# Performance work log

Measured on AMD Instinct MI355X. Metric: run time of the kernel, lower is better.

The kernel has to match this reference:

```python
import jax, jax.numpy as jnp
import numpy as np

DIM = 64; NH = 8; WS = 8; B = 8; H = 128; W = 128
HD = DIM // NH
SCALE = HD ** -0.5
BN_S = np.float32(1.0 / np.sqrt(1.0 + 1e-5))  # eval-mode BatchNorm with running mean=0, var=1


def conv2d(x, w, stride=1, padding=0, groups=1, bias=None):
    out = jax.lax.conv_general_dilated(
        x, w, (stride, stride), [(padding, padding), (padding, padding)],
        dimension_numbers=('NCHW', 'OIHW', 'NCHW'), feature_group_count=groups)
    if bias is not None:
        out = out + bias[None, :, None, None]
    return out


def bn(x, g, b):
    return x * (g * BN_S)[None, :, None, None] + b[None, :, None, None]


def maxpool(x, k, s):
    return jax.lax.reduce_window(x, -jnp.inf, jax.lax.max, (1, 1, k, k), (1, 1, s, s), 'VALID')


def avgpool(x, kh, kw, ph, pw):
    # torch AvgPool2d: zero padding, count_include_pad=True -> divide by full kernel size
    s = jax.lax.reduce_window(x, 0.0, jax.lax.add, (1, 1, kh, kw), (1, 1, 1, 1),
                              [(0, 0), (0, 0), (ph, ph), (pw, pw)])
    return s / (kh * kw)


def fft_h(x):
    # high-pass: zero magnitude within radius 40 of the shifted spectrum center
    h, w = x.shape[-2], x.shape[-1]
    f = jnp.fft.fftshift(jnp.fft.fft2(x), axes=(-2, -1))
    ii = jnp.arange(h)[:, None] - h // 2
    jj = jnp.arange(w)[None, :] - w // 2
    mask = (jnp.sqrt((ii * ii + jj * jj).astype(jnp.float32)) > 40.0).astype(x.dtype)
    filt = f * (jnp.abs(f) * mask)
    return jnp.abs(jnp.fft.ifft2(jnp.fft.ifftshift(filt, axes=(-2, -1))))


def gabor_branch(x, f_cos, f_sin, gb_b1, gb_b2, gb_w, w_post, g_post, b_post,
                 w_gc, b_gc, w_gc1, b_gc1, w_gc2, b_gc2):
    xs = x.shape[2]  # x_size (square input assumed, as in the torch code)
    xc = jnp.concatenate([conv2d(x, f_cos, bias=gb_b1), conv2d(x, f_sin, bias=gb_b2)], axis=1)
    wts = jax.nn.relu(gb_w)
    fw = wts / (jnp.sum(wts) + 1e-8)
    xc = fw[0] * fft_h(xc) + fw[1] * xc
    xc = jnp.clip(bn(conv2d(xc, w_post, padding=1), g_post, b_post), 0.0, 6.0)  # ReLU6
    xc = maxpool(xc, 2, 1)
    xc = jax.nn.relu(conv2d(xc, w_gc, stride=2, bias=b_gc))
    xc = maxpool(xc, 2, 2)
    xc = jax.image.resize(xc, (xc.shape[0], xc.shape[1], xs, xs), method='bilinear')
    xc = jax.nn.relu(conv2d(xc, w_gc1, padding=1, bias=b_gc1))
    xc = conv2d(xc, w_gc2, bias=b_gc2)
    return jax.nn.log_softmax(xc, axis=1)


def forward(x, w_qkv, w_l1, g_l1, b_l1, w_l2, g_l2, b_l2, f_cos, f_sin, gb_b1, gb_b2, gb_w,
            w_post, g_post, b_post, w_gc, b_gc, w_gc1, b_gc1, w_gc2, b_gc2,
            rpb_table, w_dw, g_proj, b_proj, w_pw, rel_index):
    b, c, hh, ww = x.shape
    # local branch
    local = bn(conv2d(x, w_l2), g_l2, b_l2) + bn(conv2d(x, w_l1, padding=1), g_l1, b_l1)
    local = gabor_branch(local, f_cos, f_sin, gb_b1, gb_b2, gb_w, w_post, g_post, b_post,
                         w_gc, b_gc, w_gc1, b_gc1, w_gc2, b_gc2)
    # global branch (H, W multiples of WS -> self.pad is a no-op)
    qkv = conv2d(x, w_qkv)  # [b, 3C, H, W]
    gh, gw = hh // WS, ww // WS
    t = qkv.reshape(b, 3, NH, HD, gh, WS, gw, WS)
    t = t.transpose(1, 0, 4, 6, 2, 5, 7, 3).reshape(3, b * gh * gw, NH, WS * WS, HD)
    q, k, v = t[0], t[1], t[2]
    rpb = rpb_table[rel_index.reshape(-1)].reshape(WS * WS, WS * WS, NH).transpose(2, 0, 1)
    dots = jnp.einsum('bhid,bhjd->bhij', q, k) * SCALE + rpb[None]
    attn = jax.nn.softmax(dots, axis=-1)
    o = jnp.einsum('bhij,bhjd->bhid', attn, v)
    o = o.reshape(b, gh, gw, NH, WS, WS, HD).transpose(0, 3, 6, 1, 4, 2, 5).reshape(b, c, hh, ww)
    # directional reflect-pad + avg pool (kernel (8,1)/(1,8), stride 1, pad 3)
    ox = avgpool(jnp.pad(o, ((0, 0), (0, 0), (0, 1), (0, 0)), mode='reflect'), WS, 1, WS // 2 - 1, 0)
    oy = avgpool(jnp.pad(o, ((0, 0), (0, 0), (0, 0), (0, 1)), mode='reflect'), 1, WS, 0, WS // 2 - 1)
    out = ox + oy + local
    out = jnp.pad(out, ((0, 0), (0, 0), (0, 1), (0, 1)))  # pad_out
    out = conv2d(bn(conv2d(out, w_dw, padding=(WS - 1) // 2, groups=c), g_proj, b_proj), w_pw)
    return out[:, :, :hh, :ww]


def _gabor(sig, th, lam, psi, gam, ks, use_cos):
    half = (ks - 1) // 2
    y, x = np.meshgrid(np.arange(-half, half + 1), np.arange(-half, half + 1))
    x = x.astype(np.float32); y = y.astype(np.float32)
    sx = sig[..., None, None]; sy = (sig / gam)[..., None, None]
    t = th[..., None, None]; l = lam[..., None, None]; p = psi[..., None, None]
    xt = x * np.cos(t) + y * np.sin(t)
    yt = -x * np.sin(t) + y * np.cos(t)
    env = np.exp(-0.5 * (xt ** 2 / sx ** 2 + yt ** 2 / sy ** 2))
    car = np.cos(2.0 * np.pi / l * xt + p) if use_cos else np.sin(2.0 * np.pi / l * xt + p)
    return (env * car).astype(np.float32)


def setup_inputs() -> dict:
    rng = np.random.default_rng(0)
    def rn(*s, sc=0.05):
        return jnp.asarray(rng.standard_normal(s).astype(np.float32) * sc)
    sig, th, lam, psi, gam = [rng.standard_normal((DIM // 2, DIM)).astype(np.float32) for _ in range(5)]
    f_cos = jnp.asarray(_gabor(sig, th, lam, psi, gam, 3, True))
    f_sin = jnp.asarray(_gabor(sig, th, lam, psi, gam, 3, False))
    coords = np.stack(np.meshgrid(np.arange(WS), np.arange(WS), indexing='ij')).reshape(2, -1)
    rel = (coords[:, :, None] - coords[:, None, :]).transpose(1, 2, 0)
    rel[:, :, 0] += WS - 1; rel[:, :, 1] += WS - 1; rel[:, :, 0] *= 2 * WS - 1
    rel_index = jnp.asarray(rel.sum(-1).astype(np.int32))  # [64, 64]
    return dict(
        x=rn(B, DIM, H, W, sc=1.0),
        w_qkv=rn(3 * DIM, DIM, 1, 1),
        w_l1=rn(DIM, DIM, 3, 3), g_l1=jnp.ones(DIM), b_l1=jnp.zeros(DIM),
        w_l2=rn(DIM, DIM, 1, 1), g_l2=jnp.ones(DIM), b_l2=jnp.zeros(DIM),
        f_cos=f_cos, f_sin=f_sin,
        gb_b1=rn(DIM // 2), gb_b2=rn(DIM // 2), gb_w=jnp.ones(2),
        w_post=rn(DIM, DIM, 3, 3), g_post=jnp.ones(DIM), b_post=jnp.zeros(DIM),
        w_gc=rn(64, 64, 3, 3), b_gc=rn(64),
        w_gc1=rn(64, 64, 3, 3), b_gc1=rn(64),
        w_gc2=rn(64, 64, 1, 1), b_gc2=rn(64),
        rpb_table=rn((2 * WS - 1) ** 2, NH, sc=0.02),
        w_dw=rn(DIM, 1, WS, WS), g_proj=jnp.ones(DIM), b_proj=jnp.zeros(DIM),
        w_pw=rn(DIM, DIM, 1, 1),
        rel_index=rel_index,
    )


def reference(x, w_qkv, w_l1, g_l1, b_l1, w_l2, g_l2, b_l2, f_cos, f_sin, gb_b1, gb_b2, gb_w,
              w_post, g_post, b_post, w_gc, b_gc, w_gc1, b_gc1, w_gc2, b_gc2,
              rpb_table, w_dw, g_proj, b_proj, w_pw, rel_index):
    return forward(x, w_qkv, w_l1, g_l1, b_l1, w_l2, g_l2, b_l2, f_cos, f_sin, gb_b1, gb_b2, gb_w,
                   w_post, g_post, b_post, w_gc, b_gc, w_gc1, b_gc1, w_gc2, b_gc2,
                   rpb_table, w_dw, g_proj, b_proj, w_pw, rel_index)
```

## Files before the change

### kernel.cpp

```cpp
#include <hip/hip_runtime.h>
#include <math.h>

#define BN_SC 0.9999950000375f
#define P2N   (6.283185307179586f / 126.f)
#define ATT_SCALE 0.35355339059327373f

typedef float v4f __attribute__((ext_vector_type(4)));
typedef short bf16x8 __attribute__((ext_vector_type(8)));
typedef float f32x4 __attribute__((ext_vector_type(4)));
typedef unsigned short u16;

enum { M_LOCAL = 0, M_GABOR = 1, M_BNRELU6 = 2, M_BIASRELU = 3 };

__device__ __forceinline__ u16 f2bf(float f) {
  unsigned u = __float_as_uint(f);
  return (u16)((u + 0x7FFFu + ((u >> 16) & 1u)) >> 16);
}
__device__ __forceinline__ float bf2f(u16 h) {
  return __uint_as_float(((unsigned)h) << 16);
}

__global__ __launch_bounds__(256) void rpbprep_k(
    const float* __restrict__ rpb, const int* __restrict__ relidx, float* __restrict__ rpbt)
{
// ... 263 lines not shown
  const int wco = wv & 1, wpx = wv >> 1;
  const int b = blockIdx.y;
  const int oy0 = (blockIdx.x >> 3) * 8, ox0 = (blockIdx.x & 7) * 8;
  const int l15 = lane & 15, l4 = lane >> 4;
  const int pr_ = l15 >> 3, pc_ = l15 & 7;
  const int aoff = l15 * 576 + l4 * 8;
  const u16* wh0 = wh + wco * 32 * 576 + aoff;
  const u16* wl0 = wl + wco * 32 * 576 + aoff;

  f32x4 acc[2][2];
#pragma unroll
  for (int f = 0; f < 2; ++f)
#pragma unroll
    for (int g = 0; g < 2; ++g) { f32x4 z = {0.f, 0.f, 0.f, 0.f}; acc[f][g] = z; }

  const int PHA[9] = {0, 0, 0, 0, 1, 1, 2, 2, 3};
  const int OYO[9] = {0, 0, 1, 1, 0, 1, 0, 0, 0};
  const int OXO[9] = {0, 1, 0, 1, 0, 0, 0, 1, 0};

#pragma unroll 1
  for (int cc = 0; cc < 64; cc += 32) {
#pragma unroll
    for (int pos = 0; pos < 9; ++pos) {
      const int ph = PHA[pos];
      if (pos == 0 || pos == 4 || pos == 6 || pos == 8) {
        __syncthreads();
        for (int e = tid; e < 648; e += 256) {
          int pix = e >> 3, part = e & 7;
          int pu = pix / 9, pv = pix - pu * 9;
          int u = oy0 + pu, v = ox0 + pv;
          uint4 val = make_uint4(0u, 0u, 0u, 0u);
          if (u < 63 && v < 63) {
            const u16* s = ((part < 4) ? ph_h : ph_l)
                + (((size_t)(b * 4 + ph) * 63 + u) * 63 + v) * 64 + cc + (part & 3) * 8;
            val = *(const uint4*)s;
          }
          *(uint4*)(lds + pix * 144 + part * 16) = val;
        }
        __syncthreads();
      }
      bf16x8 ah0 = *(const bf16x8*)(wh0 + pos * 64 + cc);
      bf16x8 al0 = *(const bf16x8*)(wl0 + pos * 64 + cc);
      bf16x8 ah1 = *(const bf16x8*)(wh0 + 16 * 576 + pos * 64 + cc);
      bf16x8 al1 = *(const bf16x8*)(wl0 + 16 * 576 + pos * 64 + cc);
#pragma unroll
      for (int g = 0; g < 2; ++g) {
        const int lrow = wpx * 4 + g * 2 + pr_ + OYO[pos];
        const int lcol = pc_ + OXO[pos];
        const char* pb = lds + (lrow * 9 + lcol) * 144 + l4 * 16;
        bf16x8 bh = *(const bf16x8*)pb;
        bf16x8 bl = *(const bf16x8*)(pb + 64);
        acc[0][g] = __builtin_amdgcn_mfma_f32_16x16x32_bf16(ah0, bh, acc[0][g], 0, 0, 0);
        acc[1][g] = __builtin_amdgcn_mfma_f32_16x16x32_bf16(ah1, bh, acc[1][g], 0, 0, 0);
        acc[0][g] = __builtin_amdgcn_mfma_f32_16x16x32_bf16(ah0, bl, acc[0][g], 0, 0, 0);
        acc[0][g] = __builtin_amdgcn_mfma_f32_16x16x32_bf16(al0, bh, acc[0][g], 0, 0, 0);
        acc[1][g] = __builtin_amdgcn_mfma_f32_16x16x32_bf16(ah1, bl, acc[1][g], 0, 0, 0);
        acc[1][g] = __builtin_amdgcn_mfma_f32_16x16x32_bf16(al1, bh, acc[1][g], 0, 0, 0);
      }
    }
  }

  const int ox = ox0 + pc_;
#pragma unroll
  for (int f = 0; f < 2; ++f) {
    const int cb = wco * 32 + f * 16 + l4 * 4;
#pragma unroll
    for (int g = 0; g < 2; ++g) {
      int oy = oy0 + wpx * 4 + g * 2 + pr_;
      if (oy >= 62 || ox >= 62) continue;
#pragma unroll
      for (int j = 0; j < 4; ++j) {
        float v = acc[f][g][j] + bias[cb + j];
        out[(((size_t)(b * 64) + cb + j) * 62 + oy) * 62 + ox] = fmaxf(v, 0.f);
      }
    }
  }
}


__global__ __launch_bounds__(256)
void dft_rows_fwd_mf(const float* __restrict__ in, float* __restrict__ outC,
                     const u16* __restrict__ th, const u16* __restrict__ tl, int planeBase)
{
  __shared__ char lds[64 * 528];
  const int tid = threadIdx.x;
  const int lane = tid & 63;
  const int wv = __builtin_amdgcn_readfirstlane(tid >> 6);
  const int l15 = lane & 15, l4 = lane >> 4;
  const int lp = blockIdx.x >> 1, rb = (blockIdx.x & 1) * 64;
  const float* src = in + (size_t)(planeBase + lp) * 15876;

  for (int e = tid; e < 8192; e += 256) {
    int row = e >> 7, k = e & 127;
    int gr = rb + row;
    float v = (gr < 126 && k < 126) ? src[(size_t)gr * 126 + k] : 0.f;
    u16 h = f2bf(v);
    char* p = lds + row * 528 + k * 2;
    *(u16*)p = h;
    *(u16*)(p + 256) = f2bf(v - bf2f(h));
  }
  __syncthreads();

  f32x4 acc[8];
#pragma unroll
  for (int nf = 0; nf < 8; ++nf) { f32x4 z = {0.f, 0.f, 0.f, 0.f}; acc[nf] = z; }
#pragma unroll
  for (int cc = 0; cc < 128; cc += 32) {
    const char* pb = lds + (wv * 16 + l15) * 528 + cc * 2 + l4 * 16;
    bf16x8 bh = *(const bf16x8*)pb;
    bf16x8 bl = *(const bf16x8*)(pb + 256);
#pragma unroll
    for (int nf = 0; nf < 8; ++nf) {
      const int ao = (nf * 16 + l15) * 128 + cc + l4 * 8;
      bf16x8 ah = *(const bf16x8*)(th + ao);
      bf16x8 al = *(const bf16x8*)(tl + ao);
      acc[nf] = __builtin_amdgcn_mfma_f32_16x16x32_bf16(ah, bh, acc[nf], 0, 0, 0);
      acc[nf] = __builtin_amdgcn_mfma_f32_16x16x32_bf16(ah, bl, acc[nf], 0, 0, 0);
      acc[nf] = __builtin_amdgcn_mfma_f32_16x16x32_bf16(al, bh, acc[nf], 0, 0, 0);
    }
  }
  const int row = rb + wv * 16 + l15;
  if (row < 126) {
    float* o = outC + (size_t)lp * 16128 + (size_t)row * 128;
#pragma unroll
    for (int nf = 0; nf < 8; ++nf)
      *(f32x4*)(o + nf * 16 + l4 * 4) = acc[nf];
  }
}

template<bool FWD>
__global__ __launch_bounds__(256)
void dft_cols_mf(const float* __restrict__ inC, float* __restrict__ outC,
                 const u16* __restrict__ tch, const u16* __restrict__ tcl,
                 const u16* __restrict__ tsh, const u16* __restrict__ tsl)
{
  __shared__ char lds[33792];
  const int tid = threadIdx.x;
  const int lane = tid & 63;
  const int wv = __builtin_amdgcn_readfirstlane(tid >> 6);
  const int l15 = lane & 15, l4 = lane >> 4;
  const int lp = blockIdx.x >> 1, gbase = (blockIdx.x & 1) * 32;
  const float2* src = (const float2*)(inC + (size_t)lp * 16128);

  for (int e = tid; e < 4096; e += 256) {
    int col = e >> 7, k = e & 127;
    float2 v = make_float2(0.f, 0.f);
    if (k < 126) v = src[k * 64 + gbase + col];
    u16 hr = f2bf(v.x);
    u16 hi2 = f2bf(v.y);
    char* pr = lds + col * 528 + k * 2;
    char* pi = lds + 16896 + col * 528 + k * 2;
    *(u16*)pr = hr;        *(u16*)(pr + 256) = f2bf(v.x - bf2f(hr));
    *(u16*)pi = hi2;       *(u16*)(pi + 256) = f2bf(v.y - bf2f(hi2));
  }
  __syncthreads();

  f32x4 aRc[2][2], aRs[2][2], aIc[2][2], aIs[2][2];
#pragma unroll
  for (int a = 0; a < 2; ++a)
#pragma unroll
    for (int c = 0; c < 2; ++c) {
      f32x4 z = {0.f, 0.f, 0.f, 0.f};
      aRc[a][c] = z; aRs[a][c] = z; aIc[a][c] = z; aIs[a][c] = z;
    }

#pragma unroll
  for (int cc = 0; cc < 128; cc += 32) {
    bf16x8 brh[2], brl[2], bih[2], bil[2];
#pragma unroll
    for (int cf = 0; cf < 2; ++cf) {
      const char* pr = lds + (cf * 16 + l15) * 528 + cc * 2 + l4 * 16;
      brh[cf] = *(const bf16x8*)pr;
      brl[cf] = *(const bf16x8*)(pr + 256);
      const char* pi = lds + 16896 + (cf * 16 + l15) * 528 + cc * 2 + l4 * 16;
      bih[cf] = *(const bf16x8*)pi;
      bil[cf] = *(const bf16x8*)(pi + 256);
    }
#pragma unroll
    for (int chf = 0; chf < 2; ++chf) {
      const int ao = (wv * 32 + chf * 16 + l15) * 128 + cc + l4 * 8;
      bf16x8 ach = *(const bf16x8*)(tch + ao);
      bf16x8 acl = *(const bf16x8*)(tcl + ao);
      bf16x8 ash = *(const bf16x8*)(tsh + ao);
      bf16x8 asl = *(const bf16x8*)(tsl + ao);
#pragma unroll
      for (int cf = 0; cf < 2; ++cf) {
        aRc[chf][cf] = __builtin_amdgcn_mfma_f32_16x16x32_bf16(ach, brh[cf], aRc[chf][cf], 0, 0, 0);
        aRc[chf][cf] = __builtin_amdgcn_mfma_f32_16x16x32_bf16(ach, brl[cf], aRc[chf][cf], 0, 0, 0);
        aRc[chf][cf] = __builtin_amdgcn_mfma_f32_16x16x32_bf16(acl, brh[cf], aRc[chf][cf], 0, 0, 0);
        aRs[chf][cf] = __builtin_amdgcn_mfma_f32_16x16x32_bf16(ash, bih[cf], aRs[chf][cf], 0, 0, 0);
        aRs[chf][cf] = __builtin_amdgcn_mfma_f32_16x16x32_bf16(ash, bil[cf], aRs[chf][cf], 0, 0, 0);
        aRs[chf][cf] = __builtin_amdgcn_mfma_f32_16x16x32_bf16(asl, bih[cf], aRs[chf][cf], 0, 0, 0);
        aIc[chf][cf] = __builtin_amdgcn_mfma_f32_16x16x32_bf16(ach, bih[cf], aIc[chf][cf], 0, 0, 0);
        aIc[chf][cf] = __builtin_amdgcn_mfma_f32_16x16x32_bf16(ach, bil[cf], aIc[chf][cf], 0, 0, 0);
        aIc[chf][cf] = __builtin_amdgcn_mfma_f32_16x16x32_bf16(acl, bih[cf], aIc[chf][cf], 0, 0, 0);
        aIs[chf][cf] = __builtin_amdgcn_mfma_f32_16x16x32_bf16(ash, brh[cf], aIs[chf][cf], 0, 0, 0);
        aIs[chf][cf] = __builtin_amdgcn_mfma_f32_16x16x32_bf16(ash, brl[cf], aIs[chf][cf], 0, 0, 0);
        aIs[chf][cf] = __builtin_amdgcn_mfma_f32_16x16x32_bf16(asl, brh[cf], aIs[chf][cf], 0, 0, 0);
      }
    }
  }

  float2* dst = (float2*)(outC + (size_t)lp * 16128);
#pragma unroll
  for (int chf = 0; chf < 2; ++chf)
#pragma unroll
    for (int cf = 0; cf < 2; ++cf) {
      const int col = gbase + cf * 16 + l15;
      const int chb = wv * 32 + chf * 16 + l4 * 4;
#pragma unroll
      for (int j = 0; j < 4; ++j) {
        int ch = chb + j;
        if (ch >= 126) continue;
        float Cr, Ci;
        if (FWD) { Cr = aRc[chf][cf][j] + aRs[chf][cf][j]; Ci = aIc[chf][cf][j] - aIs[chf][cf][j]; }
        else     { Cr = aRc[chf][cf][j] - aRs[chf][cf][j]; Ci = aIc[chf][cf][j] + aIs[chf][cf][j]; }
        if (FWD) {
          int f1 = (ch <= 62) ? ch : ch - 126;
          int f2 = (col <= 62) ? col : col - 126;
          float sa = (f1 * f1 + f2 * f2 > 1600)
                       ? sqrtf(Cr * Cr + Ci * Ci) * (1.f / 15876.f) : 0.f;
          Cr *= sa; Ci *= sa;
        }
        dst[(size_t)ch * 64 + col] = make_float2(Cr, Ci);
      }
    }
}

__global__ __launch_bounds__(256)
void dft_rows_inv_mix_mf(const float* __restrict__ inC, const float* __restrict__ xc0,
                         const float* __restrict__ gb_w,
                         const u16* __restrict__ th, const u16* __restrict__ tl,
                         float* __restrict__ out, int planeBase)
{
  __shared__ char lds[64 * 528];
  const int tid = threadIdx.x;
  const int lane = tid & 63;
  const int wv = __builtin_amdgcn_readfirstlane(tid >> 6);
  const int l15 = lane & 15, l4 = lane >> 4;
  const int lp = blockIdx.x >> 1, rb = (blockIdx.x & 1) * 64;
  const float* src = inC + (size_t)lp * 16128;

  for (int e = tid; e < 8192; e += 256) {
    int row = e >> 7, k = e & 127;
    int gr = rb + row;
    float v = (gr < 126) ? src[(size_t)gr * 128 + k] : 0.f;
    u16 h = f2bf(v);
    char* p = lds + row * 528 + k * 2;
    *(u16*)p = h;
    *(u16*)(p + 256) = f2bf(v - bf2f(h));
  }
  __syncthreads();

  f32x4 acc[8];
#pragma unroll
  for (int nf = 0; nf < 8; ++nf) { f32x4 z = {0.f, 0.f, 0.f, 0.f}; acc[nf] = z; }
#pragma unroll
  for (int cc = 0; cc < 128; cc += 32) {
    const char* pb = lds + (wv * 16 + l15) * 528 + cc * 2 + l4 * 16;
    bf16x8 bh = *(const bf16x8*)pb;
    bf16x8 bl = *(const bf16x8*)(pb + 256);
#pragma unroll
    for (int nf = 0; nf < 8; ++nf) {
      const int ao = (nf * 16 + l15) * 128 + cc + l4 * 8;
      bf16x8 ah = *(const bf16x8*)(th + ao);
      bf16x8 al = *(const bf16x8*)(tl + ao);
      acc[nf] = __builtin_amdgcn_mfma_f32_16x16x32_bf16(ah, bh, acc[nf], 0, 0, 0);
      acc[nf] = __builtin_amdgcn_mfma_f32_16x16x32_bf16(ah, bl, acc[nf], 0, 0, 0);
      acc[nf] = __builtin_amdgcn_mfma_f32_16x16x32_bf16(al, bh, acc[nf], 0, 0, 0);
    }
  }
  const int row = rb + wv * 16 + l15;
  if (row < 126) {
    float w0 = fmaxf(gb_w[0], 0.f), w1 = fmaxf(gb_w[1], 0.f);
    float iv = 1.f / (w0 + w1 + 1e-8f);
    const float w0i = w0 * iv, w1i = w1 * iv;
    size_t base = (size_t)(planeBase + lp) * 15876 + (size_t)row * 126;
#pragma unroll
    for (int nf = 0; nf < 8; ++nf) {
      const int n20 = nf * 16 + l4 * 4;
#pragma unroll
      for (int j = 0; j < 4; ++j) {
        int n2 = n20 + j;
        if (n2 < 126)
          out[base + n2] = w0i * fabsf(acc[nf][j]) + w1i * xc0[base + n2];
      }
    }
  }
}

__global__ __launch_bounds__(256) void mp2_k(const float* __restrict__ in, float* __restrict__ out)
{
  int idx = blockIdx.x * 256 + threadIdx.x;
  if (idx >= 512 * 31 * 31) return;
  int x = idx % 31, y = (idx / 31) % 31, p = idx / 961;
  const float* ip = in + (size_t)p * 3844 + (size_t)(2 * y) * 62 + 2 * x;
  out[idx] = fmaxf(fmaxf(ip[0], ip[1]), fmaxf(ip[62], ip[63]));
}

__global__ __launch_bounds__(256)
void resize_bf_k(const float* __restrict__ in, u16* __restrict__ xh, u16* __restrict__ xl)
{
  int idx = blockIdx.x * 256 + threadIdx.x;
  if (idx >= 2097152) return;
  int cg = idx & 15, x = (idx >> 4) & 127, y = (idx >> 11) & 127, b = idx >> 18;
  float sy = (y + 0.5f) * (31.f / 128.f) - 0.5f; sy = fminf(fmaxf(sy, 0.f), 30.f);
  float sx = (x + 0.5f) * (31.f / 128.f) - 0.5f; sx = fminf(fmaxf(sx, 0.f), 30.f);
  int y0 = (int)sy; float fy = sy - (float)y0; int y1 = min(y0 + 1, 30);
  int x0 = (int)sx; float fx = sx - (float)x0; int x1 = min(x0 + 1, 30);
  const float* base = in + (size_t)(b * 64 + cg * 4) * 961;
  ushort4 hv, lv;
#pragma unroll
  for (int k = 0; k < 4; ++k) {
    const float* ip = base + k * 961;
    float v = (1.f - fy) * ((1.f - fx) * ip[y0 * 31 + x0] + fx * ip[y0 * 31 + x1])
            + fy         * ((1.f - fx) * ip[y1 * 31 + x0] + fx * ip[y1 * 31 + x1]);
    u16 h = f2bf(v);
    ((u16*)&hv)[k] = h;
    ((u16*)&lv)[k] = f2bf(v - bf2f(h));
  }
  size_t o = (((size_t)b * 128 + y) * 128 + x) * 64 + cg * 4;
  *(ushort4*)(xh + o) = hv;
  *(ushort4*)(xl + o) = lv;
}

__global__ __launch_bounds__(256)
void pwlsm_mf(const u16* __restrict__ xh, const u16* __restrict__ xl,
              const u16* __restrict__ wh, const u16* __restrict__ wl,
              const float* __restrict__ bias, float* __restrict__ out)
{
  __shared__ char lds[17664];
  const int tid = threadIdx.x;
  const int lane = tid & 63;
  const int wv = __builtin_amdgcn_readfirstlane(tid >> 6);
  const int l15 = lane & 15, l4 = lane >> 4;
  const size_t px0 = (size_t)blockIdx.x * 64;

  for (int e = tid; e < 1024; e += 256) {
    int pix = e >> 4, part = e & 15;
    const u16* s = ((part < 8) ? xh : xl) + (px0 + pix) * 64 + (part & 7) * 8;
    char* d = lds + pix * 272 + ((part < 8) ? part * 16 : 128 + (part - 8) * 16);
    *(uint4*)d = *(const uint4*)s;
  }
  __syncthreads();

  f32x4 acc[4];
#pragma unroll
  for (int p = 0; p < 4; ++p) { f32x4 z = {0.f, 0.f, 0.f, 0.f}; acc[p] = z; }
  const int co16 = wv * 16;
  const u16* wa = wh + (size_t)(co16 + l15) * 64 + l4 * 8;
  const u16* wb = wl + (size_t)(co16 + l15) * 64 + l4 * 8;
#pragma unroll
  for (int cc = 0; cc < 64; cc += 32) {
    bf16x8 ah = *(const bf16x8*)(wa + cc);
    bf16x8 al = *(const bf16x8*)(wb + cc);
#pragma unroll
    for (int p = 0; p < 4; ++p) {
      const char* pb = lds + (16 * p + l15) * 272 + cc * 2 + l4 * 16;
      bf16x8 bh = *(const bf16x8*)pb;
      bf16x8 bl = *(const bf16x8*)(pb + 128);
      acc[p] = __builtin_amdgcn_mfma_f32_16x16x32_bf16(ah, bh, acc[p], 0, 0, 0);
      acc[p] = __builtin_amdgcn_mfma_f32_16x16x32_bf16(ah, bl, acc[p], 0, 0, 0);
      acc[p] = __builtin_amdgcn_mfma_f32_16x16x32_bf16(al, bh, acc[p], 0, 0, 0);
    }
  }
  float4 bv = *(const float4*)&bias[co16 + l4 * 4];
  __syncthreads();
  float* zs = (float*)lds;
// ... 77 lines not shown
void attn_mf_k(const float* __restrict__ x, const u16* __restrict__ wqh,
               const u16* __restrict__ wql, const float* __restrict__ rpbt,
               float* __restrict__ o_out)
{
  __shared__ uint4 lds4[3200];
  char* lds = (char*)lds4;
  const int tid = threadIdx.x;
  const int lane = tid & 63;
  const int wv = __builtin_amdgcn_readfirstlane(tid >> 6);
  const int b = blockIdx.x >> 8, gy = (blockIdx.x >> 4) & 15, gx = blockIdx.x & 15;
  const int y0 = gy * 8, x0 = gx * 8;
  const int l15 = lane & 15, l4 = lane >> 4;

  for (int e = tid; e < 4096; e += 256) {
    int cin = e >> 6, pix = e & 63;
    float v = x[((size_t)(b * 64 + cin) * 128 + (y0 + (pix >> 3))) * 128 + x0 + (pix & 7)];
    u16 h = f2bf(v);
    *(u16*)(lds + pix * 272 + cin * 2)       = h;
    *(u16*)(lds + pix * 272 + 128 + cin * 2) = f2bf(v - bf2f(h));
  }
  __syncthreads();

  f32x4 acc[3][4];
#pragma unroll
  for (int r = 0; r < 3; ++r)
#pragma unroll
    for (int p = 0; p < 4; ++p) { f32x4 z = {0.f, 0.f, 0.f, 0.f}; acc[r][p] = z; }
  const u16* wa = wqh + (size_t)(48 * wv + l15) * 64 + l4 * 8;
  const u16* wb = wql + (size_t)(48 * wv + l15) * 64 + l4 * 8;
#pragma unroll
  for (int cc = 0; cc < 64; cc += 32) {
    bf16x8 bh[4], bl[4];
#pragma unroll
    for (int p = 0; p < 4; ++p) {
      const char* pb = lds + (16 * p + l15) * 272 + cc * 2 + l4 * 16;
      bh[p] = *(const bf16x8*)pb;
      bl[p] = *(const bf16x8*)(pb + 128);
    }
#pragma unroll
    for (int r = 0; r < 3; ++r) {
      bf16x8 ah = *(const bf16x8*)(wa + r * 1024 + cc);
      bf16x8 al = *(const bf16x8*)(wb + r * 1024 + cc);
#pragma unroll
      for (int p = 0; p < 4; ++p) {
        acc[r][p] = __builtin_amdgcn_mfma_f32_16x16x32_bf16(ah, bh[p], acc[r][p], 0, 0, 0);
        acc[r][p] = __builtin_amdgcn_mfma_f32_16x16x32_bf16(ah, bl[p], acc[r][p], 0, 0, 0);
        acc[r][p] = __builtin_amdgcn_mfma_f32_16x16x32_bf16(al, bh[p], acc[r][p], 0, 0, 0);
      }
    }
  }
  __syncthreads();

#pragma unroll
  for (int r = 0; r < 3; ++r) {
    const int ch0 = 48 * wv + 16 * r + l4 * 4;
#pragma unroll
    for (int p = 0; p < 4; ++p) {
      const int pix = 16 * p + l15;
      if (ch0 < 64) {
#pragma unroll
        for (int j = 0; j < 4; ++j)
          *(float*)(lds + ((ch0 + j) * 65 + pix) * 4) = acc[r][p][j];
      } else {
        const int col = (ch0 < 128) ? (ch0 - 64) : (64 + ch0 - 128);
        *(f32x4*)(lds + 17408 + pix * 528 + col * 4) = acc[r][p];
      }
    }
  }
  __syncthreads();

  const int row = y0 + (lane >> 3), col = x0 + (lane & 7);
  const int h0 = wv, h1 = wv + 4;
  float q0[8], q1[8];
#pragma unroll
  for (int d = 0; d < 8; ++d) {
    q0[d] = *(const float*)(lds + ((h0 * 8 + d) * 65 + lane) * 4);
    q1[d] = *(const float*)(lds + ((h1 * 8 + d) * 65 + lane) * 4);
  }
  const float* rb0 = rpbt + h0 * 4096;
  const float* rb1 = rpbt + h1 * 4096;
  float P0[64], P1[64];
#pragma unroll
  for (int j = 0; j < 64; ++j) { P0[j] = rb0[j * 64 + lane]; P1[j] = rb1[j * 64 + lane]; }
  float m0 = -1e30f, m1 = -1e30f;
#pragma unroll
  for (int j = 0; j < 64; ++j) {
    const char* kp = lds + 17408 + j * 528;
    float4 a0 = *(const float4*)(kp + (h0 * 8) * 4);
    float4 a1 = *(const float4*)(kp + (h0 * 8) * 4 + 16);
    float4 b0 = *(const float4*)(kp + (h1 * 8) * 4);
    float4 b1 = *(const float4*)(kp + (h1 * 8) * 4 + 16);
    float s0 = q0[0] * a0.x + q0[1] * a0.y + q0[2] * a0.z + q0[3] * a0.w
             + q0[4] * a1.x + q0[5] * a1.y + q0[6] * a1.z + q0[7] * a1.w;
    float s1 = q1[0] * b0.x + q1[1] * b0.y + q1[2] * b0.z + q1[3] * b0.w
             + q1[4] * b1.x + q1[5] * b1.y + q1[6] * b1.z + q1[7] * b1.w;
    s0 = s0 * ATT_SCALE + P0[j];
    s1 = s1 * ATT_SCALE + P1[j];
    P0[j] = s0; P1[j] = s1;
    m0 = fmaxf(m0, s0); m1 = fmaxf(m1, s1);
  }
  float sum0 = 0.f, sum1 = 0.f;
#pragma unroll
  for (int j = 0; j < 64; ++j) {
    float p0 = __expf(P0[j] - m0); P0[j] = p0; sum0 += p0;
    float p1 = __expf(P1[j] - m1); P1[j] = p1; sum1 += p1;
  }
  float inv0 = 1.f / sum0, inv1 = 1.f / sum1;

  float acc0[8], acc1[8];
#pragma unroll
  for (int d = 0; d < 8; ++d) { acc0[d] = 0.f; acc1[d] = 0.f; }
#pragma unroll
  for (int j = 0; j < 64; ++j) {
    const char* vp = lds + 17408 + j * 528 + 256;
    float p0 = P0[j], p1 = P1[j];
    float4 v00 = *(const float4*)(vp + (h0 * 8) * 4);
    float4 v01 = *(const float4*)(vp + (h0 * 8) * 4 + 16);
    float4 v10 = *(const float4*)(vp + (h1 * 8) * 4);
    float4 v11 = *(const float4*)(vp + (h1 * 8) * 4 + 16);
    acc0[0] += p0 * v00.x; acc0[1] += p0 * v00.y; acc0[2] += p0 * v00.z; acc0[3] += p0 * v00.w;
    acc0[4] += p0 * v01.x; acc0[5] += p0 * v01.y; acc0[6] += p0 * v01.z; acc0[7] += p0 * v01.w;
    acc1[0] += p1 * v10.x; acc1[1] += p1 * v10.y; acc1[2] += p1 * v10.z; acc1[3] += p1 * v10.w;
    acc1[4] += p1 * v11.x; acc1[5] += p1 * v11.y; acc1[6] += p1 * v11.z; acc1[7] += p1 * v11.w;
  }
#pragma unroll
  for (int d = 0; d < 8; ++d) {
    o_out[((size_t)(b * 64 + h0 * 8 + d) * 128 + row) * 128 + col] = acc0[d] * inv0;
    o_out[((size_t)(b * 64 + h1 * 8 + d) * 128 + row) * 128 + col] = acc1[d] * inv1;
  }
}

__global__ __launch_bounds__(256)
void avgadd_k(const float* __restrict__ o, const float* __restrict__ loc, float* __restrict__ out)
{
  __shared__ float t[24][128];
  const int tid = threadIdx.x;
  const int y0 = blockIdx.x * 16;
  const size_t p = blockIdx.y;
  const float* op = o + (p << 14);
  for (int e = tid; e < 24 * 128; e += 256) {
    int rr = e >> 7, x = e & 127;
    int r = y0 - 3 + rr;
    float v = 0.f;
    if (r >= 0 && r <= 128) { int r2 = (r == 128) ? 126 : r; v = op[r2 * 128 + x]; }
    t[rr][x] = v;
  }
  __syncthreads();
#pragma unroll
  for (int k = 0; k < 8; ++k) {
    int idx = k * 256 + tid;
    int ly = idx >> 7, x = idx & 127;
    float s1 = 0.f;
#pragma unroll
    for (int tt = 0; tt < 8; ++tt) s1 += t[ly + tt][x];
    float s2 = 0.f;
#pragma unroll
    for (int tt = 0; tt < 8; ++tt) {
      int cc = x - 3 + tt;
      if (cc >= 0 && cc <= 128) { int ss = (cc == 128) ? 126 : cc; s2 += t[ly + 3][ss]; }
    }
    size_t gi = (p << 14) + (size_t)(y0 + ly) * 128 + x;
    out[gi] = 0.125f * (s1 + s2) + loc[gi];
  }
}

__global__ __launch_bounds__(256)
void dw_k(const float* __restrict__ in, const float* __restrict__ w,
          const float* __restrict__ g, const float* __restrict__ bb, float* __restrict__ out)
{
  __shared__ float t[23 * 23];
  const int tid = threadIdx.x;
  const int tx = tid & 15, ty = tid >> 4;
  const int x0 = blockIdx.x * 16, y0 = blockIdx.y * 16;
  const int pc = blockIdx.z;
  const int c = pc & 63;
  const float* ip = in + (size_t)pc * 16384;
  for (int e = tid; e < 529; e += 256) {
    int yy = e / 23, xx = e % 23;
    int iy = y0 + yy - 3, ix = x0 + xx - 3;
    t[e] = (iy >= 0 && iy < 128 && ix >= 0 && ix < 128) ? ip[iy * 128 + ix] : 0.f;
  }
  __syncthreads();
  const float* wk = w + c * 64;
  float s = 0.f;
#pragma unroll
  for (int ky = 0; ky < 8; ++ky)
#pragma unroll
    for (int kx = 0; kx < 8; ++kx)
      s += t[(ty + ky) * 23 + tx + kx] * wk[ky * 8 + kx];
  out[(size_t)pc * 16384 + (y0 + ty) * 128 + x0 + tx] = s * (g[c] * BN_SC) + bb[c];
}

extern "C" void kernel_launch(void* const* d_in, const int* in_sizes, int n_in,
                              void* d_out, int out_size, void* d_ws, size_t ws_size,
                              hipStream_t stream)
{
  const float* x      = (const float*)d_in[0];
  const float* w_qkv  = (const float*)d_in[1];
  const float* w_l1   = (const float*)d_in[2];
  const float* g_l1   = (const float*)d_in[3];
  const float* b_l1   = (const float*)d_in[4];
  const float* w_l2   = (const float*)d_in[5];
  const float* g_l2   = (const float*)d_in[6];
  const float* b_l2   = (const float*)d_in[7];
  const float* f_cos  = (const float*)d_in[8];
  const float* f_sin  = (const float*)d_in[9];
  const float* gb_b1  = (const float*)d_in[10];
  const float* gb_b2  = (const float*)d_in[11];
  const float* gb_w   = (const float*)d_in[12];
  const float* w_post = (const float*)d_in[13];
  const float* g_post = (const float*)d_in[14];
  const float* b_post = (const float*)d_in[15];
  const float* w_gc   = (const float*)d_in[16];
  const float* b_gc   = (const float*)d_in[17];
  const float* w_gc1  = (const float*)d_in[18];
  const float* b_gc1  = (const float*)d_in[19];
  const float* w_gc2  = (const float*)d_in[20];
  const float* b_gc2  = (const float*)d_in[21];
  const float* rpb    = (const float*)d_in[22];
  const float* w_dw   = (const float*)d_in[23];
  const float* g_proj = (const float*)d_in[24];
  const float* b_proj = (const float*)d_in[25];
  const float* w_pw   = (const float*)d_in[26];
  const int*   relidx = (const int*)d_in[27];
  float* out = (float*)d_out;

  char* ws = (char*)d_ws;
  float* R1   = (float*)(ws + 0);
  float* R2   = (float*)(ws + 33554432);
  float* R3   = (float*)(ws + 67108864);
  float* C1   = R3;
  float* C2   = (float*)(ws + 83623936);
  float* XC5  = (float*)(ws + 100139008);
  float* RPBT = (float*)(ws + 102107136);
  u16* XH_A = (u16*)(ws + 33554432);
  u16* XL_A = (u16*)(ws + 33554432 + 16777216);
  u16* XH_B = (u16*)(ws + 67108864);
  u16* XL_B = (u16*)(ws + 83886080);
  u16* PH_H = (u16*)(ws + 0);
  u16* PH_L = (u16*)(ws + 16257024);
  u16* XC7H = (u16*)(ws + 0);
  u16* XC7L = (u16*)(ws + 16777216);
  u16* TB   = (u16*)(ws + 100139008);
  u16* WH   = (u16*)(ws + 100663296);
  u16* WL   = (u16*)(ws + 100745216);
  float* BLS = (float*)(ws + 100827136);
  u16* WQH  = (u16*)(ws + 100827392);
  u16* WQL  = (u16*)(ws + 100851968);
  u16* WGH  = (u16*)(ws + 100876544);
  u16* WGL  = (u16*)(ws + 100884736);
  u16* WPH  = (u16*)(ws + 100892928);
  u16* WPL  = (u16*)(ws + 100901120);

  rpbprep_k<<<128, 256, 0, stream>>>(rpb, relidx, RPBT);

  wsplit_k<<<144, 256, 0, stream>>>(w_l1, g_l1, WH, WL, 64, 9, 0, 0, 10);
  wsplit_k<<<16, 256, 0, stream>>>(w_l2, g_l2, WH, WL, 64, 1, 0, 9, 10);
  bls_k<<<1, 64, 0, stream>>>(b_l1, b_l2, BLS);
  xsplit_k<128><<<1024, 256, 0, stream>>>(x, XH_A, XL_A);
  convmf_k<M_LOCAL, 10, 128, 128, 1, true><<<dim3(64, 8), 256, 0, stream>>>(
      XH_A, XL_A, WH, WL, BLS, nullptr, nullptr, XH_B, XL_B);

  wsplit_k<<<72, 256, 0, stream>>>(f_cos, nullptr, WH, WL, 32, 9, 0, 0, 9);
  wsplit_k<<<72, 256, 0, stream>>>(f_sin, nullptr, WH, WL, 32, 9, 32, 0, 9);
  convmf_k<M_GABOR, 9, 128, 126, 0, false><<<dim3(64, 8), 256, 0, stream>>>(
      XH_B, XL_B, WH, WL, gb_b1, gb_b2, R2, nullptr, nullptr);

  tprep_k<<<256, 256, 0, stream>>>(TB);
  for (int chunk = 0; chunk < 2; ++chunk) {
    int pb = chunk * 256;
    dft_rows_fwd_mf<<<512, 256, 0, stream>>>(R2, C1, TB, TB + 16384, pb);
    dft_cols_mf<true><<<512, 256, 0, stream>>>(C1, C2, TB + 32768, TB + 49152,
                                               TB + 65536, TB + 81920);
    dft_cols_mf<false><<<512, 256, 0, stream>>>(C2, C1, TB + 32768, TB + 49152,
                                                TB + 65536, TB + 81920);
    dft_rows_inv_mix_mf<<<512, 256, 0, stream>>>(C1, R2, gb_w, TB + 98304, TB + 114688,
                                                 R1, pb);
  }

  wsplit_k<<<144, 256, 0, stream>>>(w_post, g_post, WH, WL, 64, 9, 0, 0, 9);
  xsplit_k<126><<<1008, 256, 0, stream>>>(R1, XH_B, XL_B);
  convmf_k<M_BNRELU6, 9, 126, 126, 1, false><<<dim3(64, 8), 256, 0, stream>>>(
      XH_B, XL_B, WH, WL, b_post, nullptr, R2, nullptr, nullptr);

  mpsplit_k<<<1008, 256, 0, stream>>>(R2, PH_H, PH_L);

  wsplit_gc_k<<<144, 256, 0, stream>>>(w_gc, WH, WL);
  convgc_mf<<<dim3(64, 8), 256, 0, stream>>>(PH_H, PH_L, WH, WL, b_gc, R3);

  mp2_k<<<1922, 256, 0, stream>>>(R3, XC5);
  resize_bf_k<<<8192, 256, 0, stream>>>(XC5, XH_B, XL_B);

  wsplit_k<<<48, 256, 0, stream>>>(w_qkv, nullptr, WQH, WQL, 192, 1, 0, 0, 1);
  wsplit_k<<<16, 256, 0, stream>>>(w_gc2, nullptr, WGH, WGL, 64, 1, 0, 0, 1);
  wsplit_k<<<16, 256, 0, stream>>>(w_pw, nullptr, WPH, WPL, 64, 1, 0, 0, 1);

  wsplit_k<<<144, 256, 0, stream>>>(w_gc1, nullptr, WH, WL, 64, 9, 0, 0, 9);
  convmf_k<M_BIASRELU, 9, 128, 128, 1, true><<<dim3(64, 8), 256, 0, stream>>>(
      XH_B, XL_B, WH, WL, b_gc1, nullptr, nullptr, XC7H, XC7L);

  pwlsm_mf<<<2048, 256, 0, stream>>>(XC7H, XC7L, WGH, WGL, b_gc2, R2);
  attn_mf_k<<<2048, 256, 0, stream>>>(x, WQH, WQL, RPBT, R1);
  avgadd_k<<<dim3(8, 512), 256, 0, stream>>>(R1, R2, R3);
  dw_k<<<dim3(8, 8, 512), 256, 0, stream>>>(R3, w_dw, g_proj, b_proj, R2);
  pw_mf<<<2048, 256, 0, stream>>>(R2, WPH, WPL, out);
  (void)in_sizes; (void)n_in; (void)out_size; (void)ws_size;
}
```

Baseline: 830.9 us.

## Split DFT kernels into finer blocks and break max/sum dependency chains in attention

The four DFT matrix-multiply kernels now give each block half as many rows or columns of a plane, doubling the grid from 512 to 1024 blocks and halving LDS and accumulator registers per block. This aims to raise occupancy and parallelism on a GPU with many compute units. The cost is that twiddle-table fragments are reloaded by more blocks and each wave issues fewer MFMAs per LDS load. Separately, the attention softmax splits its running max and sum into even/odd accumulators to shorten serial dependency chains.

```diff
diff --git a/kernel.cpp b/kernel.cpp
--- a/kernel.cpp
+++ b/kernel.cpp
@@ -369,15 +369,15 @@
 void dft_rows_fwd_mf(const float* __restrict__ in, float* __restrict__ outC,
                      const u16* __restrict__ th, const u16* __restrict__ tl, int planeBase)
 {
-  __shared__ char lds[64 * 528];
+  __shared__ char lds[32 * 528];
   const int tid = threadIdx.x;
   const int lane = tid & 63;
   const int wv = __builtin_amdgcn_readfirstlane(tid >> 6);
   const int l15 = lane & 15, l4 = lane >> 4;
-  const int lp = blockIdx.x >> 1, rb = (blockIdx.x & 1) * 64;
+  const int lp = blockIdx.x >> 2, rb = (blockIdx.x & 3) * 32;
   const float* src = in + (size_t)(planeBase + lp) * 15876;
 
-  for (int e = tid; e < 8192; e += 256) {
+  for (int e = tid; e < 4096; e += 256) {
     int row = e >> 7, k = e & 127;
     int gr = rb + row;
     float v = (gr < 126 && k < 126) ? src[(size_t)gr * 126 + k] : 0.f;
@@ -388,30 +388,31 @@
   }
   __syncthreads();
 
-  f32x4 acc[8];
-#pragma unroll
-  for (int nf = 0; nf < 8; ++nf) { f32x4 z = {0.f, 0.f, 0.f, 0.f}; acc[nf] = z; }
+  const int rg = wv & 1, nh = wv >> 1;
+  f32x4 acc[4];
+#pragma unroll
+  for (int f = 0; f < 4; ++f) { f32x4 z = {0.f, 0.f, 0.f, 0.f}; acc[f] = z; }
 #pragma unroll
   for (int cc = 0; cc < 128; cc += 32) {
-    const char* pb = lds + (wv * 16 + l15) * 528 + cc * 2 + l4 * 16;
+    const char* pb = lds + (rg * 16 + l15) * 528 + cc * 2 + l4 * 16;
     bf16x8 bh = *(const bf16x8*)pb;
     bf16x8 bl = *(const bf16x8*)(pb + 256);
 #pragma unroll
-    for (int nf = 0; nf < 8; ++nf) {
-      const int ao = (nf * 16 + l15) * 128 + cc + l4 * 8;
+    for (int f = 0; f < 4; ++f) {
+      const int ao = ((nh * 4 + f) * 16 + l15) * 128 + cc + l4 * 8;
       bf16x8 ah = *(const bf16x8*)(th + ao);
       bf16x8 al = *(const bf16x8*)(tl + ao);
-      acc[nf] = __builtin_amdgcn_mfma_f32_16x16x32_bf16(ah, bh, acc[nf], 0, 0, 0);
-      acc[nf] = __builtin_amdgcn_mfma_f32_16x16x32_bf16(ah, bl, acc[nf], 0, 0, 0);
-      acc[nf] = __builtin_amdgcn_mfma_f32_16x16x32_bf16(al, bh, acc[nf], 0, 0, 0);
-    }
-  }
-  const int row = rb + wv * 16 + l15;
+      acc[f] = __builtin_amdgcn_mfma_f32_16x16x32_bf16(ah, bh, acc[f], 0, 0, 0);
+      acc[f] = __builtin_amdgcn_mfma_f32_16x16x32_bf16(ah, bl, acc[f], 0, 0, 0);
+      acc[f] = __builtin_amdgcn_mfma_f32_16x16x32_bf16(al, bh, acc[f], 0, 0, 0);
+    }
+  }
+  const int row = rb + rg * 16 + l15;
   if (row < 126) {
     float* o = outC + (size_t)lp * 16128 + (size_t)row * 128;
 #pragma unroll
-    for (int nf = 0; nf < 8; ++nf)
-      *(f32x4*)(o + nf * 16 + l4 * 4) = acc[nf];
+    for (int f = 0; f < 4; ++f)
+      *(f32x4*)(o + (nh * 4 + f) * 16 + l4 * 4) = acc[f];
   }
 }
 
@@ -421,48 +422,42 @@
                  const u16* __restrict__ tch, const u16* __restrict__ tcl,
                  const u16* __restrict__ tsh, const u16* __restrict__ tsl)
 {
-  __shared__ char lds[33792];
+  __shared__ char lds[16896];
   const int tid = threadIdx.x;
   const int lane = tid & 63;
   const int wv = __builtin_amdgcn_readfirstlane(tid >> 6);
   const int l15 = lane & 15, l4 = lane >> 4;
-  const int lp = blockIdx.x >> 1, gbase = (blockIdx.x & 1) * 32;
+  const int lp = blockIdx.x >> 2, gbase = (blockIdx.x & 3) * 16;
   const float2* src = (const float2*)(inC + (size_t)lp * 16128);
 
-  for (int e = tid; e < 4096; e += 256) {
+  for (int e = tid; e < 2048; e += 256) {
     int col = e >> 7, k = e & 127;
     float2 v = make_float2(0.f, 0.f);
     if (k < 126) v = src[k * 64 + gbase + col];
     u16 hr = f2bf(v.x);
     u16 hi2 = f2bf(v.y);
     char* pr = lds + col * 528 + k * 2;
-    char* pi = lds + 16896 + col * 528 + k * 2;
+    char* pi = lds + 8448 + col * 528 + k * 2;
     *(u16*)pr = hr;        *(u16*)(pr + 256) = f2bf(v.x - bf2f(hr));
     *(u16*)pi = hi2;       *(u16*)(pi + 256) = f2bf(v.y - bf2f(hi2));
   }
   __syncthreads();
 
-  f32x4 aRc[2][2], aRs[2][2], aIc[2][2], aIs[2][2];
-#pragma unroll
-  for (int a = 0; a < 2; ++a)
-#pragma unroll
-    for (int c = 0; c < 2; ++c) {
-      f32x4 z = {0.f, 0.f, 0.f, 0.f};
-      aRc[a][c] = z; aRs[a][c] = z; aIc[a][c] = z; aIs[a][c] = z;
-    }
+  f32x4 aRc[2], aRs[2], aIc[2], aIs[2];
+#pragma unroll
+  for (int a = 0; a < 2; ++a) {
+    f32x4 z = {0.f, 0.f, 0.f, 0.f};
+    aRc[a] = z; aRs[a] = z; aIc[a] = z; aIs[a] = z;
+  }
 
 #pragma unroll
   for (int cc = 0; cc < 128; cc += 32) {
-    bf16x8 brh[2], brl[2], bih[2], bil[2];
-#pragma unroll
-    for (int cf = 0; cf < 2; ++cf) {
-      const char* pr = lds + (cf * 16 + l15) * 528 + cc * 2 + l4 * 16;
-      brh[cf] = *(const bf16x8*)pr;
-      brl[cf] = *(const bf16x8*)(pr + 256);
-      const char* pi = lds + 16896 + (cf * 16 + l15) * 528 + cc * 2 + l4 * 16;
-      bih[cf] = *(const bf16x8*)pi;
-      bil[cf] = *(const bf16x8*)(pi + 256);
-    }
+    const char* pr = lds + l15 * 528 + cc * 2 + l4 * 16;
+    bf16x8 brh = *(const bf16x8*)pr;
+    bf16x8 brl = *(const bf16x8*)(pr + 256);
+    const char* pi = lds + 8448 + l15 * 528 + cc * 2 + l4 * 16;
+    bf16x8 bih = *(const bf16x8*)pi;
+    bf16x8 bil = *(const bf16x8*)(pi + 256);
 #pragma unroll
     for (int chf = 0; chf < 2; ++chf) {
       const int ao = (wv * 32 + chf * 16 + l15) * 128 + cc + l4 * 8;
@@ -470,48 +465,43 @@
       bf16x8 acl = *(const bf16x8*)(tcl + ao);
       bf16x8 ash = *(const bf16x8*)(tsh + ao);
       bf16x8 asl = *(const bf16x8*)(tsl + ao);
-#pragma unroll
-      for (int cf = 0; cf < 2; ++cf) {
-        aRc[chf][cf] = __builtin_amdgcn_mfma_f32_16x16x32_bf16(ach, brh[cf], aRc[chf][cf], 0, 0, 0);
-        aRc[chf][cf] = __builtin_amdgcn_mfma_f32_16x16x32_bf16(ach, brl[cf], aRc[chf][cf], 0, 0, 0);
-        aRc[chf][cf] = __builtin_amdgcn_mfma_f32_16x16x32_bf16(acl, brh[cf], aRc[chf][cf], 0, 0, 0);
-        aRs[chf][cf] = __builtin_amdgcn_mfma_f32_16x16x32_bf16(ash, bih[cf], aRs[chf][cf], 0, 0, 0);
-        aRs[chf][cf] = __builtin_amdgcn_mfma_f32_16x16x32_bf16(ash, bil[cf], aRs[chf][cf], 0, 0, 0);
-        aRs[chf][cf] = __builtin_amdgcn_mfma_f32_16x16x32_bf16(asl, bih[cf], aRs[chf][cf], 0, 0, 0);
-        aIc[chf][cf] = __builtin_amdgcn_mfma_f32_16x16x32_bf16(ach, bih[cf], aIc[chf][cf], 0, 0, 0);
-        aIc[chf][cf] = __builtin_amdgcn_mfma_f32_16x16x32_bf16(ach, bil[cf], aIc[chf][cf], 0, 0, 0);
-        aIc[chf][cf] = __builtin_amdgcn_mfma_f32_16x16x32_bf16(acl, bih[cf], aIc[chf][cf], 0, 0, 0);
-        aIs[chf][cf] = __builtin_amdgcn_mfma_f32_16x16x32_bf16(ash, brh[cf], aIs[chf][cf], 0, 0, 0);
-        aIs[chf][cf] = __builtin_amdgcn_mfma_f32_16x16x32_bf16(ash, brl[cf], aIs[chf][cf], 0, 0, 0);
-        aIs[chf][cf] = __builtin_amdgcn_mfma_f32_16x16x32_bf16(asl, brh[cf], aIs[chf][cf], 0, 0, 0);
+      aRc[chf] = __builtin_amdgcn_mfma_f32_16x16x32_bf16(ach, brh, aRc[chf], 0, 0, 0);
+      aRc[chf] = __builtin_amdgcn_mfma_f32_16x16x32_bf16(ach, brl, aRc[chf], 0, 0, 0);
+      aRc[chf] = __builtin_amdgcn_mfma_f32_16x16x32_bf16(acl, brh, aRc[chf], 0, 0, 0);
+      aRs[chf] = __builtin_amdgcn_mfma_f32_16x16x32_bf16(ash, bih, aRs[chf], 0, 0, 0);
+      aRs[chf] = __builtin_amdgcn_mfma_f32_16x16x32_bf16(ash, bil, aRs[chf], 0, 0, 0);
+      aRs[chf] = __builtin_amdgcn_mfma_f32_16x16x32_bf16(asl, bih, aRs[chf], 0, 0, 0);
+      aIc[chf] = __builtin_amdgcn_mfma_f32_16x16x32_bf16(ach, bih, aIc[chf], 0, 0, 0);
+      aIc[chf] = __builtin_amdgcn_mfma_f32_16x16x32_bf16(ach, bil, aIc[chf], 0, 0, 0);
+      aIc[chf] = __builtin_amdgcn_mfma_f32_16x16x32_bf16(acl, bih, aIc[chf], 0, 0, 0);
+      aIs[chf] = __builtin_amdgcn_mfma_f32_16x16x32_bf16(ash, brh, aIs[chf], 0, 0, 0);
+      aIs[chf] = __builtin_amdgcn_mfma_f32_16x16x32_bf16(ash, brl, aIs[chf], 0, 0, 0);
+      aIs[chf] = __builtin_amdgcn_mfma_f32_16x16x32_bf16(asl, brh, aIs[chf], 0, 0, 0);
+    }
+  }
+
+  float2* dst = (float2*)(outC + (size_t)lp * 16128);
+  const int col = gbase + l15;
+#pragma unroll
+  for (int chf = 0; chf < 2; ++chf) {
+    const int chb = wv * 32 + chf * 16 + l4 * 4;
+#pragma unroll
+    for (int j = 0; j < 4; ++j) {
+      int ch = chb + j;
+      if (ch >= 126) continue;
+      float Cr, Ci;
+      if (FWD) { Cr = aRc[chf][j] + aRs[chf][j]; Ci = aIc[chf][j] - aIs[chf][j]; }
+      else     { Cr = aRc[chf][j] - aRs[chf][j]; Ci = aIc[chf][j] + aIs[chf][j]; }
+      if (FWD) {
+        int f1 = (ch <= 62) ? ch : ch - 126;
+        int f2 = (col <= 62) ? col : col - 126;
+        float sa = (f1 * f1 + f2 * f2 > 1600)
+                     ? sqrtf(Cr * Cr + Ci * Ci) * (1.f / 15876.f) : 0.f;
+        Cr *= sa; Ci *= sa;
       }
-    }
-  }
-
-  float2* dst = (float2*)(outC + (size_t)lp * 16128);
-#pragma unroll
-  for (int chf = 0; chf < 2; ++chf)
-#pragma unroll
-    for (int cf = 0; cf < 2; ++cf) {
-      const int col = gbase + cf * 16 + l15;
-      const int chb = wv * 32 + chf * 16 + l4 * 4;
-#pragma unroll
-      for (int j = 0; j < 4; ++j) {
-        int ch = chb + j;
-        if (ch >= 126) continue;
-        float Cr, Ci;
-        if (FWD) { Cr = aRc[chf][cf][j] + aRs[chf][cf][j]; Ci = aIc[chf][cf][j] - aIs[chf][cf][j]; }
-        else     { Cr = aRc[chf][cf][j] - aRs[chf][cf][j]; Ci = aIc[chf][cf][j] + aIs[chf][cf][j]; }
-        if (FWD) {
-          int f1 = (ch <= 62) ? ch : ch - 126;
-          int f2 = (col <= 62) ? col : col - 126;
-          float sa = (f1 * f1 + f2 * f2 > 1600)
-                       ? sqrtf(Cr * Cr + Ci * Ci) * (1.f / 15876.f) : 0.f;
-          Cr *= sa; Ci *= sa;
-        }
-        dst[(size_t)ch * 64 + col] = make_float2(Cr, Ci);
-      }
-    }
+      dst[(size_t)ch * 64 + col] = make_float2(Cr, Ci);
+    }
+  }
 }
 
 __global__ __launch_bounds__(256)
@@ -520,15 +510,15 @@
                          const u16* __restrict__ th, const u16* __restrict__ tl,
                          float* __restrict__ out, int planeBase)
 {
-  __shared__ char lds[64 * 528];
+  __shared__ char lds[32 * 528];
   const int tid = threadIdx.x;
   const int lane = tid & 63;
   const int wv = __builtin_amdgcn_readfirstlane(tid >> 6);
   const int l15 = lane & 15, l4 = lane >> 4;
-  const int lp = blockIdx.x >> 1, rb = (blockIdx.x & 1) * 64;
+  const int lp = blockIdx.x >> 2, rb = (blockIdx.x & 3) * 32;
   const float* src = inC + (size_t)lp * 16128;
 
-  for (int e = tid; e < 8192; e += 256) {
+  for (int e = tid; e < 4096; e += 256) {
     int row = e >> 7, k = e & 127;
     int gr = rb + row;
     float v = (gr < 126) ? src[(size_t)gr * 128 + k] : 0.f;
@@ -539,38 +529,39 @@
   }
   __syncthreads();
 
-  f32x4 acc[8];
-#pragma unroll
-  for (int nf = 0; nf < 8; ++nf) { f32x4 z = {0.f, 0.f, 0.f, 0.f}; acc[nf] = z; }
+  const int rg = wv & 1, nh = wv >> 1;
+  f32x4 acc[4];
+#pragma unroll
+  for (int f = 0; f < 4; ++f) { f32x4 z = {0.f, 0.f, 0.f, 0.f}; acc[f] = z; }
 #pragma unroll
   for (int cc = 0; cc < 128; cc += 32) {
-    const char* pb = lds + (wv * 16 + l15) * 528 + cc * 2 + l4 * 16;
+    const char* pb = lds + (rg * 16 + l15) * 528 + cc * 2 + l4 * 16;
     bf16x8 bh = *(const bf16x8*)pb;
     bf16x8 bl = *(const bf16x8*)(pb + 256);
 #pragma unroll
-    for (int nf = 0; nf < 8; ++nf) {
-      const int ao = (nf * 16 + l15) * 128 + cc + l4 * 8;
+    for (int f = 0; f < 4; ++f) {
+      const int ao = ((nh * 4 + f) * 16 + l15) * 128 + cc + l4 * 8;
       bf16x8 ah = *(const bf16x8*)(th + ao);
       bf16x8 al = *(const bf16x8*)(tl + ao);
-      acc[nf] = __builtin_amdgcn_mfma_f32_16x16x32_bf16(ah, bh, acc[nf], 0, 0, 0);
-      acc[nf] = __builtin_amdgcn_mfma_f32_16x16x32_bf16(ah, bl, acc[nf], 0, 0, 0);
-      acc[nf] = __builtin_amdgcn_mfma_f32_16x16x32_bf16(al, bh, acc[nf], 0, 0, 0);
-    }
-  }
-  const int row = rb + wv * 16 + l15;
+      acc[f] = __builtin_amdgcn_mfma_f32_16x16x32_bf16(ah, bh, acc[f], 0, 0, 0);
+      acc[f] = __builtin_amdgcn_mfma_f32_16x16x32_bf16(ah, bl, acc[f], 0, 0, 0);
+      acc[f] = __builtin_amdgcn_mfma_f32_16x16x32_bf16(al, bh, acc[f], 0, 0, 0);
+    }
+  }
+  const int row = rb + rg * 16 + l15;
   if (row < 126) {
     float w0 = fmaxf(gb_w[0], 0.f), w1 = fmaxf(gb_w[1], 0.f);
     float iv = 1.f / (w0 + w1 + 1e-8f);
     const float w0i = w0 * iv, w1i = w1 * iv;
     size_t base = (size_t)(planeBase + lp) * 15876 + (size_t)row * 126;
 #pragma unroll
-    for (int nf = 0; nf < 8; ++nf) {
-      const int n20 = nf * 16 + l4 * 4;
+    for (int f = 0; f < 4; ++f) {
+      const int n20 = (nh * 4 + f) * 16 + l4 * 4;
 #pragma unroll
       for (int j = 0; j < 4; ++j) {
         int n2 = n20 + j;
         if (n2 < 126)
-          out[base + n2] = w0i * fabsf(acc[nf][j]) + w1i * xc0[base + n2];
+          out[base + n2] = w0i * fabsf(acc[f][j]) + w1i * xc0[base + n2];
       }
     }
   }
@@ -814,7 +805,7 @@
   float P0[64], P1[64];
 #pragma unroll
   for (int j = 0; j < 64; ++j) { P0[j] = rb0[j * 64 + lane]; P1[j] = rb1[j * 64 + lane]; }
-  float m0 = -1e30f, m1 = -1e30f;
+  float m0a = -1e30f, m0b = -1e30f, m1a = -1e30f, m1b = -1e30f;
 #pragma unroll
   for (int j = 0; j < 64; ++j) {
     const char* kp = lds + 17408 + j * 528;
@@ -829,15 +820,19 @@
     s0 = s0 * ATT_SCALE + P0[j];
     s1 = s1 * ATT_SCALE + P1[j];
     P0[j] = s0; P1[j] = s1;
-    m0 = fmaxf(m0, s0); m1 = fmaxf(m1, s1);
-  }
-  float sum0 = 0.f, sum1 = 0.f;
+    if (j & 1) { m0b = fmaxf(m0b, s0); m1b = fmaxf(m1b, s1); }
+    else       { m0a = fmaxf(m0a, s0); m1a = fmaxf(m1a, s1); }
+  }
+  float m0 = fmaxf(m0a, m0b), m1 = fmaxf(m1a, m1b);
+  float s0a = 0.f, s0b = 0.f, s1a = 0.f, s1b = 0.f;
 #pragma unroll
   for (int j = 0; j < 64; ++j) {
-    float p0 = __expf(P0[j] - m0); P0[j] = p0; sum0 += p0;
-    float p1 = __expf(P1[j] - m1); P1[j] = p1; sum1 += p1;
-  }
-  float inv0 = 1.f / sum0, inv1 = 1.f / sum1;
+    float p0 = __expf(P0[j] - m0); P0[j] = p0;
+    float p1 = __expf(P1[j] - m1); P1[j] = p1;
+    if (j & 1) { s0b += p0; s1b += p1; }
+    else       { s0a += p0; s1a += p1; }
+  }
+  float inv0 = 1.f / (s0a + s0b), inv1 = 1.f / (s1a + s1b);
 
   float acc0[8], acc1[8];
 #pragma unroll
@@ -1001,13 +996,13 @@
   tprep_k<<<256, 256, 0, stream>>>(TB);
   for (int chunk = 0; chunk < 2; ++chunk) {
     int pb = chunk * 256;
-    dft_rows_fwd_mf<<<512, 256, 0, stream>>>(R2, C1, TB, TB + 16384, pb);
-    dft_cols_mf<true><<<512, 256, 0, stream>>>(C1, C2, TB + 32768, TB + 49152,
-                                               TB + 65536, TB + 81920);
-    dft_cols_mf<false><<<512, 256, 0, stream>>>(C2, C1, TB + 32768, TB + 49152,
+    dft_rows_fwd_mf<<<1024, 256, 0, stream>>>(R2, C1, TB, TB + 16384, pb);
+    dft_cols_mf<true><<<1024, 256, 0, stream>>>(C1, C2, TB + 32768, TB + 49152,
                                                 TB + 65536, TB + 81920);
-    dft_rows_inv_mix_mf<<<512, 256, 0, stream>>>(C1, R2, gb_w, TB + 98304, TB + 114688,
-                                                 R1, pb);
+    dft_cols_mf<false><<<1024, 256, 0, stream>>>(C2, C1, TB + 32768, TB + 49152,
+                                                 TB + 65536, TB + 81920);
+    dft_rows_inv_mix_mf<<<1024, 256, 0, stream>>>(C1, R2, gb_w, TB + 98304, TB + 114688,
+                                                  R1, pb);
   }
 
   wsplit_k<<<144, 256, 0, stream>>>(w_post, g_post, WH, WL, 64, 9, 0, 0, 9);
```

New measurement: 868.8 us. 1.05x slower.
